# Performance work log

Hardware: AMD Instinct MI355X
Metric: run time of the kernel (lower is better)

## Reference

```python
import jax, jax.numpy as jnp
import numpy as np

D_I = 1024
D_O = 1024
B = 4
S = 4096

def setup_inputs() -> dict:
    key = jax.random.key(0)
    kx, kq, kk, kv = jax.random.split(key, 4)
    x = jax.random.normal(kx, (B, S, D_I), dtype=jnp.float32)
    # torch Linear(d_i, d_o) weight is [d_o, d_i]; we store transposed [d_i, d_o]
    sc = 1.0 / np.sqrt(D_I)
    Wq = jax.random.uniform(kq, (D_I, D_O), jnp.float32, -sc, sc)
    Wk = jax.random.uniform(kk, (D_I, D_O), jnp.float32, -sc, sc)
    Wv = jax.random.uniform(kv, (D_I, D_O), jnp.float32, -sc, sc)
    return {"x": x, "Wq": Wq, "Wk": Wk, "Wv": Wv}

def reference(x, Wq, Wk, Wv):
    # x: [B, S, d_i]
    q = jnp.einsum('bsd,de->bse', x, Wq)  # [B,S,d_o]
    k = jnp.einsum('bsd,de->bse', x, Wk)
    v = jnp.einsum('bsd,de->bse', x, Wv)
    scores = jnp.einsum('bqe,bke->bqk', q, k)  # [B,S,S]
    S_len = x.shape[1]
    causal = jnp.tril(jnp.ones((S_len, S_len), dtype=bool))  # keep lower tri
    scores = jnp.where(causal[None], scores, -jnp.inf)
    attn = jax.nn.softmax(scores / jnp.sqrt(jnp.float32(v.shape[-1])), axis=-1)
    # dropout p=0.0 -> identity
    return jnp.einsum('bqk,bke->bqe', attn, v)  # [B,S,d_o]
```

## Files before the change

### kernel.cpp

```cpp
#include <hip/hip_runtime.h>

typedef __bf16 bf16x8 __attribute__((ext_vector_type(8)));
typedef float f32x4 __attribute__((ext_vector_type(4)));

#define B_SZ 4
#define S_SZ 4096
#define D_SZ 1024
#define ELEMS_MAT ((size_t)B_SZ * S_SZ * D_SZ)

#define OFF_Q  ((size_t)0)
#define OFF_K  (ELEMS_MAT)
#define OFF_VT (2 * ELEMS_MAT)
#define ZONE   (3 * ELEMS_MAT)
#define OFF_XB (ZONE)
#define OFF_V  (ZONE + ELEMS_MAT)
#define OFF_WT (ZONE + 2 * ELEMS_MAT)
#define OFF_S  (ZONE)
#define S_BATCH ((size_t)8912896)

#define MFMA16(a, b, c) __builtin_amdgcn_mfma_f32_16x16x32_bf16((a), (b), (c), 0, 0, 0)

static __device__ __forceinline__ unsigned short f2bf(float f) {
  __bf16 h = (__bf16)f;
  return __builtin_bit_cast(unsigned short, h);
}

static __device__ __forceinline__ void async_lds16(const void* g, void* l) {
  __builtin_amdgcn_global_load_lds((__attribute__((address_space(1))) void*)g,
                                   (__attribute__((address_space(3))) void*)l, 16, 0, 0);
}

__global__ void cast_x_kernel(const float* __restrict__ x, unsigned short* __restrict__ xb) {
  size_t i = ((size_t)blockIdx.x * 256 + threadIdx.x) * 8;
  f32x4 a = *(const f32x4*)(x + i);
  f32x4 b = *(const f32x4*)(x + i + 4);
  bf16x8 o;
  o[0] = (__bf16)a[0]; o[1] = (__bf16)a[1]; o[2] = (__bf16)a[2]; o[3] = (__bf16)a[3];
  o[4] = (__bf16)b[0]; o[5] = (__bf16)b[1]; o[6] = (__bf16)b[2]; o[7] = (__bf16)b[3];
  *(bf16x8*)(xb + i) = o;
}

__global__ void cast_wt_kernel(const float* __restrict__ Wq, const float* __restrict__ Wk,
                               const float* __restrict__ Wv, unsigned short* __restrict__ Wt) {
  __shared__ float tl[64][65];
  const float* W = blockIdx.z == 0 ? Wq : (blockIdx.z == 1 ? Wk : Wv);
  unsigned short* out = Wt + (size_t)blockIdx.z * (size_t)D_SZ * (size_t)D_SZ;
  const int k0 = blockIdx.x * 64, n0 = blockIdx.y * 64;
  const int t = threadIdx.x;
  for (int i = t; i < 4096; i += 256) {
    int r = i >> 6, c = i & 63;
    tl[r][c] = W[(size_t)(k0 + r) * D_SZ + n0 + c];
  }
  __syncthreads();
  for (int i = t; i < 4096; i += 256) {
    int r = i >> 6, c = i & 63;
    out[(size_t)(n0 + r) * D_SZ + k0 + c] = f2bf(tl[c][r]);
  }
}

static __device__ __forceinline__ void stage_tile(const char* Asrc, size_t lda,
                                                  const char* Bsrc, size_t ldb,
                                                  unsigned short* ldsA, unsigned short* ldsB,
                                                  int tid) {
#pragma unroll
  for (int it = 0; it < 4; ++it) {
    int i = it * 512 + tid;
    int row = i >> 3;
    int scol = ((i & 7) ^ (row & 7)) << 4;
    async_lds16(Asrc + (size_t)row * lda + scol, (char*)ldsA + i * 16);
  }
#pragma unroll
  for (int it = 0; it < 4; ++it) {
    int i = it * 512 + tid;
    int row = i >> 3;
    int scol = ((i & 7) ^ (row & 7)) << 4;
    async_lds16(Bsrc + (size_t)row * ldb + scol, (char*)ldsB + i * 16);
  }
}

static __device__ __forceinline__ void compute_tile(const unsigned short* As,
                                                    const unsigned short* Bs,
                                                    int wm, int wn, int lr, int hi,
                                                    f32x4 acc[8][4]) {
  const char* Ab = (const char*)As;
  const char* Bb = (const char*)Bs;
#pragma unroll
  for (int q = 0; q < 4; ++q) {
    const int qm = q >> 1, qn = q & 1;
    bf16x8 af[4][2], bfr[2][2];
#pragma unroll
    for (int f = 0; f < 4; ++f) {
      const int r = wm * 128 + (qm * 4 + f) * 16 + lr;
#pragma unroll
      for (int kk = 0; kk < 2; ++kk)
        af[f][kk] = *(const bf16x8*)(Ab + r * 128 + ((kk * 64 + hi * 16) ^ ((r & 7) << 4)));
    }
#pragma unroll
    for (int f = 0; f < 2; ++f) {
      const int r = wn * 64 + (qn * 2 + f) * 16 + lr;
#pragma unroll
      for (int kk = 0; kk < 2; ++kk)
        bfr[f][kk] = *(const bf16x8*)(Bb + r * 128 + ((kk * 64 + hi * 16) ^ ((r & 7) << 4)));
    }
    __builtin_amdgcn_s_setprio(1);
#pragma unroll
    for (int kk = 0; kk < 2; ++kk)
#pragma unroll
      for (int f = 0; f < 4; ++f)
#pragma unroll
        for (int g = 0; g < 2; ++g)
          acc[qm * 4 + f][qn * 2 + g] = MFMA16(af[f][kk], bfr[g][kk], acc[qm * 4 + f][qn * 2 + g]);
    __builtin_amdgcn_s_setprio(0);
  }
}

static __device__ __forceinline__ void gemm_mainloop(const char* A, size_t lda,
                                                     const char* B, size_t ldb, int NT,
                                                     unsigned short sm[2][2][16384],
                                                     int tid, f32x4 acc[8][4]) {
  const int lane = tid & 63, w = tid >> 6;
  const int wm = w >> 2, wn = w & 3, lr = lane & 15, hi = lane >> 4;
  stage_tile(A, lda, B, ldb, sm[0][0], sm[0][1], tid);
  for (int t = 0; t < NT - 1; ++t) {
    const int cur = t & 1;
    stage_tile(A + (size_t)(t + 1) * 128, lda, B + (size_t)(t + 1) * 128, ldb,
               sm[cur ^ 1][0], sm[cur ^ 1][1], tid);
    asm volatile("s_waitcnt vmcnt(8)" ::: "memory");
    __builtin_amdgcn_s_barrier();
    compute_tile(sm[cur][0], sm[cur][1], wm, wn, lr, hi, acc);
    __builtin_amdgcn_s_barrier();
  }
  asm volatile("s_waitcnt vmcnt(0)" ::: "memory");
  __builtin_amdgcn_s_barrier();
  compute_tile(sm[(NT - 1) & 1][0], sm[(NT - 1) & 1][1], wm, wn, lr, hi, acc);
}

#define GEMM_PRE()                                    \
  __shared__ unsigned short sm[2][2][16384];          \
  const int tid = threadIdx.x;                        \
  f32x4 acc[8][4];                                    \
  {                                                   \
    const f32x4 z4 = {0.f, 0.f, 0.f, 0.f};            \
    _Pragma("unroll") for (int f = 0; f < 8; ++f)     \
      _Pragma("unroll") for (int g = 0; g < 4; ++g)   \
        acc[f][g] = z4;                               \
  }

#define EPI_IDX()                                     \
  const int lane = tid & 63, w = tid >> 6;            \
  const int wm = w >> 2, wn = w & 3;                  \
  const int lr = lane & 15, hi = lane >> 4;

__global__ __launch_bounds__(512, 2) void gemm_qkv256(const unsigned short* __restrict__ xb,
                                                      const unsigned short* __restrict__ Wt,
                                                      unsigned short* __restrict__ Q,
                                                      unsigned short* __restrict__ K,
                                                      unsigned short* __restrict__ V) {
  GEMM_PRE();
  const int bid = blockIdx.x;
  const int sw = (bid & 7) * 96 + (bid >> 3);
  const int mt = sw % 64, nt = sw / 64;
  const char* A = (const char*)xb + (size_t)mt * 256 * 2048;
  const char* Bp = (const char*)Wt + (size_t)nt * 256 * 2048;
  gemm_mainloop(A, 2048, Bp, 2048, 16, sm, tid, acc);
  EPI_IDX();
  unsigned short* Out = (nt >> 2) == 0 ? Q : ((nt >> 2) == 1 ? K : V);
  const int nb = (nt & 3) * 256;
#pragma unroll
  for (int f = 0; f < 8; ++f)
#pragma unroll
    for (int g = 0; g < 4; ++g)
#pragma unroll
      for (int j = 0; j < 4; ++j) {
        const int m = mt * 256 + wm * 128 + f * 16 + hi * 4 + j;
        const int n = nb + wn * 64 + g * 16 + lr;
        Out[(size_t)m * D_SZ + n] = f2bf(acc[f][g][j]);
      }
}

__global__ void transpose_v_kernel(const unsigned short* __restrict__ V,
                                   unsigned short* __restrict__ Vt) {
  __shared__ unsigned short tl[64][65];
  const int s0 = blockIdx.x * 64, d0 = blockIdx.y * 64, b = blockIdx.z;
  const int t = threadIdx.x;
  const unsigned short* Vb = V + (size_t)b * S_SZ * D_SZ;
  unsigned short* Vo = Vt + (size_t)b * D_SZ * S_SZ;
  for (int i = t; i < 4096; i += 256) {
    int r = i >> 6, c = i & 63;
    tl[r][c] = Vb[(size_t)(s0 + r) * D_SZ + d0 + c];
  }
  __syncthreads();
  for (int i = t; i < 4096; i += 256) {
    int r = i >> 6, c = i & 63;
    Vo[(size_t)(d0 + r) * S_SZ + s0 + c] = tl[c][r];
  }
}

__global__ __launch_bounds__(512, 2) void s_gemm256(const unsigned short* __restrict__ Q,
                                                    const unsigned short* __restrict__ K,
                                                    unsigned short* __restrict__ Sp) {
  GEMM_PRE();
  const int bid = blockIdx.x;
  const int sw = (bid & 7) * 68 + (bid >> 3);
  const int b = sw / 136;
  const int tile = sw % 136;
  int I = (int)((sqrtf(8.0f * tile + 1.0f) - 1.0f) * 0.5f);
  while ((I + 1) * (I + 2) / 2 <= tile) ++I;
  while (I * (I + 1) / 2 > tile) --I;
  const int J = tile - I * (I + 1) / 2;
  const char* A = (const char*)Q + ((size_t)b * S_SZ + (size_t)I * 256) * 2048;
  const char* Bp = (const char*)K + ((size_t)b * S_SZ + (size_t)J * 256) * 2048;
  gemm_mainloop(A, 2048, Bp, 2048, 16, sm, tid, acc);
  EPI_IDX();
  const int L = (I + 1) * 256;
  unsigned short* So = Sp + (size_t)b * S_BATCH + (size_t)(I * (I + 1) / 2) * 65536;
#pragma unroll
  for (int f = 0; f < 8; ++f)
#pragma unroll
    for (int g = 0; g < 4; ++g)
#pragma unroll
      for (int j = 0; j < 4; ++j) {
        const int m = wm * 128 + f * 16 + hi * 4 + j;
        const int n = J * 256 + wn * 64 + g * 16 + lr;
        float val = acc[f][g][j] * 0.03125f;
        if (n > I * 256 + m) val = -1e30f;
        So[(size_t)m * L + n] = f2bf(val);
      }
}

__global__ __launch_bounds__(256) void softmax_kernel(unsigned short* __restrict__ Sp) {
  const int w = threadIdx.x >> 6, lane = threadIdx.x & 63;
  const int rowflat = blockIdx.x * 4 + w;
  const int rr = 16383 - rowflat;
  const int b = rr >> 12, q = rr & 4095;
  const int I = q >> 8;
  const int L = (I + 1) << 8;
  unsigned short* base = Sp + (size_t)b * S_BATCH + (size_t)(I * (I + 1) / 2) * 65536 +
                         (size_t)(q & 255) * L;
  const int niter = (L + 511) >> 9;
  const __bf16 NEG = (__bf16)(-1e30f);
  bf16x8 v[8];
#pragma unroll
  for (int jt = 0; jt < 8; ++jt) {
    if (jt < niter) {
      const int off = jt * 512 + lane * 8;
      if (off < L) v[jt] = *(const bf16x8*)(base + off);
      else { bf16x8 fz; fz[0]=NEG;fz[1]=NEG;fz[2]=NEG;fz[3]=NEG;fz[4]=NEG;fz[5]=NEG;fz[6]=NEG;fz[7]=NEG; v[jt] = fz; }
    }
  }
  float m = -1e30f;
#pragma unroll
  for (int jt = 0; jt < 8; ++jt)
    if (jt < niter)
#pragma unroll
      for (int e = 0; e < 8; ++e) m = fmaxf(m, (float)v[jt][e]);
  m = fmaxf(m, __shfl_xor(m, 1));  m = fmaxf(m, __shfl_xor(m, 2));
  m = fmaxf(m, __shfl_xor(m, 4));  m = fmaxf(m, __shfl_xor(m, 8));
  m = fmaxf(m, __shfl_xor(m, 16)); m = fmaxf(m, __shfl_xor(m, 32));
  float l = 0.f;
#pragma unroll
  for (int jt = 0; jt < 8; ++jt)
    if (jt < niter)
#pragma unroll
      for (int e = 0; e < 8; ++e) l += __expf((float)v[jt][e] - m);
  l += __shfl_xor(l, 1);  l += __shfl_xor(l, 2);  l += __shfl_xor(l, 4);
  l += __shfl_xor(l, 8);  l += __shfl_xor(l, 16); l += __shfl_xor(l, 32);
  const float rl = 1.0f / l;
#pragma unroll
  for (int jt = 0; jt < 8; ++jt) {
    if (jt < niter) {
      const int off = jt * 512 + lane * 8;
      if (off < L) {
        bf16x8 p;
#pragma unroll
        for (int e = 0; e < 8; ++e) p[e] = (__bf16)(__expf((float)v[jt][e] - m) * rl);
        *(bf16x8*)(base + off) = p;
      }
    }
  }
}

__global__ __launch_bounds__(512, 2) void pv256(const unsigned short* __restrict__ Sp,
                                                const unsigned short* __restrict__ Vt,
                                                float* __restrict__ out) {
  GEMM_PRE();
  const int bid = blockIdx.x;
  const int sw = (bid & 7) * 32 + (bid >> 3);
  const int I = sw >> 4, b = (sw >> 2) & 3, nt = sw & 3;
  const int L = (I + 1) * 256;
  const char* A = (const char*)(Sp + (size_t)b * S_BATCH + (size_t)(I * (I + 1) / 2) * 65536);
  const char* Bp = (const char*)Vt + ((size_t)b * D_SZ + (size_t)nt * 256) * (S_SZ * 2);
  gemm_mainloop(A, (size_t)L * 2, Bp, S_SZ * 2, (I + 1) * 4, sm, tid, acc);
  EPI_IDX();
#pragma unroll
  for (int f = 0; f < 8; ++f)
#pragma unroll
    for (int g = 0; g < 4; ++g)
#pragma unroll
      for (int j = 0; j < 4; ++j) {
        const int m = wm * 128 + f * 16 + hi * 4 + j;
        const int n = nt * 256 + wn * 64 + g * 16 + lr;
        out[((size_t)b * S_SZ + (size_t)I * 256 + m) * D_SZ + n] = acc[f][g][j];
      }
}

extern "C" void kernel_launch(void* const* d_in, const int* in_sizes, int n_in,
                              void* d_out, int out_size, void* d_ws, size_t ws_size,
                              hipStream_t stream) {
  (void)in_sizes; (void)n_in; (void)out_size; (void)ws_size;
  const float* x  = (const float*)d_in[0];
  const float* Wq = (const float*)d_in[1];
  const float* Wk = (const float*)d_in[2];
  const float* Wv = (const float*)d_in[3];
  float* out = (float*)d_out;
  unsigned short* ws = (unsigned short*)d_ws;

  cast_x_kernel<<<8192, 256, 0, stream>>>(x, ws + OFF_XB);
  cast_wt_kernel<<<dim3(16, 16, 3), 256, 0, stream>>>(Wq, Wk, Wv, ws + OFF_WT);
  gemm_qkv256<<<768, 512, 0, stream>>>(ws + OFF_XB, ws + OFF_WT,
                                       ws + OFF_Q, ws + OFF_K, ws + OFF_V);
  transpose_v_kernel<<<dim3(64, 16, 4), 256, 0, stream>>>(ws + OFF_V, ws + OFF_VT);
  s_gemm256<<<544, 512, 0, stream>>>(ws + OFF_Q, ws + OFF_K, ws + OFF_S);
  softmax_kernel<<<4096, 256, 0, stream>>>(ws + OFF_S);
  pv256<<<256, 512, 0, stream>>>(ws + OFF_S, ws + OFF_VT, out);
}
```

Baseline: 404.0 us.

## Use 256x128 tiles for score GEMM and load-balance causal PV by pairing row blocks

Switches the QK^T score kernel to a new 256x128 tile mainloop, doubling the block count so the causal triangle is covered with finer granularity. The PV kernel now uses 256x128 output tiles and has each block process row block p and then 15-p sequentially, so every block does the same total K-length work instead of a skewed triangular distribution. This aims to remove tail imbalance and improve CU utilisation. In exchange it uses smaller N tiles with less reuse of A, and adds a sequential second pass per block.

New measurement: 406.3 us. Within noise of the previous version (+0.6%).

```diff
diff --git a/kernel.cpp b/kernel.cpp
--- a/kernel.cpp
+++ b/kernel.cpp
@@ -178,6 +178,84 @@
       }
 }
 
+static __device__ __forceinline__ void stage_a256(const char* src, size_t ld, char* lds, int tid) {
+#pragma unroll
+  for (int it = 0; it < 4; ++it) {
+    int i = it * 512 + tid;
+    int row = i >> 3;
+    int scol = ((i & 7) ^ (row & 7)) << 4;
+    async_lds16(src + (size_t)row * ld + scol, lds + i * 16);
+  }
+}
+static __device__ __forceinline__ void stage_b128(const char* src, size_t ld, char* lds, int tid) {
+#pragma unroll
+  for (int it = 0; it < 2; ++it) {
+    int i = it * 512 + tid;
+    int row = i >> 3;
+    int scol = ((i & 7) ^ (row & 7)) << 4;
+    async_lds16(src + (size_t)row * ld + scol, lds + i * 16);
+  }
+}
+
+static __device__ __forceinline__ void compute_tile128(const unsigned short* As,
+                                                       const unsigned short* Bs,
+                                                       int wm, int wn, int lr, int hi,
+                                                       f32x4 acc[8][2]) {
+  const char* Ab = (const char*)As;
+  const char* Bb = (const char*)Bs;
+  bf16x8 bfr[2][2];
+#pragma unroll
+  for (int g = 0; g < 2; ++g) {
+    const int r = wn * 32 + g * 16 + lr;
+#pragma unroll
+    for (int kk = 0; kk < 2; ++kk)
+      bfr[g][kk] = *(const bf16x8*)(Bb + r * 128 + ((kk * 64 + hi * 16) ^ ((r & 7) << 4)));
+  }
+#pragma unroll
+  for (int p = 0; p < 4; ++p) {
+    bf16x8 af[2][2];
+#pragma unroll
+    for (int f = 0; f < 2; ++f) {
+      const int r = wm * 128 + (p * 2 + f) * 16 + lr;
+#pragma unroll
+      for (int kk = 0; kk < 2; ++kk)
+        af[f][kk] = *(const bf16x8*)(Ab + r * 128 + ((kk * 64 + hi * 16) ^ ((r & 7) << 4)));
+    }
+    __builtin_amdgcn_s_setprio(1);
+#pragma unroll
+    for (int kk = 0; kk < 2; ++kk)
+#pragma unroll
+      for (int f = 0; f < 2; ++f)
+#pragma unroll
+        for (int g = 0; g < 2; ++g)
+          acc[p * 2 + f][g] = MFMA16(af[f][kk], bfr[g][kk], acc[p * 2 + f][g]);
+    __builtin_amdgcn_s_setprio(0);
+  }
+}
+
+static __device__ __forceinline__ void mainloop128(const char* A, size_t lda,
+                                                   const char* B, size_t ldb, int NT,
+                                                   unsigned short (*smA)[16384],
+                                                   unsigned short (*smB)[8192],
+                                                   int tid, f32x4 acc[8][2]) {
+  const int lane = tid & 63, w = tid >> 6;
+  const int wm = w >> 2, wn = w & 3, lr = lane & 15, hi = lane >> 4;
+  stage_a256(A, lda, (char*)smA[0], tid);
+  stage_b128(B, ldb, (char*)smB[0], tid);
+  for (int t = 0; t < NT - 1; ++t) {
+    const int cur = t & 1;
+    stage_a256(A + (size_t)(t + 1) * 128, lda, (char*)smA[cur ^ 1], tid);
+    stage_b128(B + (size_t)(t + 1) * 128, ldb, (char*)smB[cur ^ 1], tid);
+    asm volatile("s_waitcnt vmcnt(6)" ::: "memory");
+    __builtin_amdgcn_s_barrier();
+    compute_tile128(smA[cur], smB[cur], wm, wn, lr, hi, acc);
+    __builtin_amdgcn_s_barrier();
+  }
+  asm volatile("s_waitcnt vmcnt(0)" ::: "memory");
+  __builtin_amdgcn_s_barrier();
+  compute_tile128(smA[(NT - 1) & 1], smB[(NT - 1) & 1], wm, wn, lr, hi, acc);
+}
+
 __global__ void transpose_v_kernel(const unsigned short* __restrict__ V,
                                    unsigned short* __restrict__ Vt) {
   __shared__ unsigned short tl[64][65];
@@ -196,32 +274,43 @@
   }
 }
 
-__global__ __launch_bounds__(512, 2) void s_gemm256(const unsigned short* __restrict__ Q,
-                                                    const unsigned short* __restrict__ K,
-                                                    unsigned short* __restrict__ Sp) {
-  GEMM_PRE();
+__global__ __launch_bounds__(512, 2) void s_gemm_bn128(const unsigned short* __restrict__ Q,
+                                                       const unsigned short* __restrict__ K,
+                                                       unsigned short* __restrict__ Sp) {
+  __shared__ unsigned short smA[2][16384];
+  __shared__ unsigned short smB[2][8192];
+  const int tid = threadIdx.x;
+  f32x4 acc[8][2];
+  {
+    const f32x4 z4 = {0.f, 0.f, 0.f, 0.f};
+#pragma unroll
+    for (int f = 0; f < 8; ++f)
+#pragma unroll
+      for (int g = 0; g < 2; ++g) acc[f][g] = z4;
+  }
   const int bid = blockIdx.x;
-  const int sw = (bid & 7) * 68 + (bid >> 3);
-  const int b = sw / 136;
-  const int tile = sw % 136;
-  int I = (int)((sqrtf(8.0f * tile + 1.0f) - 1.0f) * 0.5f);
-  while ((I + 1) * (I + 2) / 2 <= tile) ++I;
-  while (I * (I + 1) / 2 > tile) --I;
-  const int J = tile - I * (I + 1) / 2;
+  const int sw = (bid & 7) * 136 + (bid >> 3);
+  const int b = sw / 272;
+  const int r = sw % 272;
+  int I = (int)((sqrtf(4.0f * r + 1.0f) - 1.0f) * 0.5f);
+  while ((I + 1) * (I + 2) <= r) ++I;
+  while (I * (I + 1) > r) --I;
+  const int Jh = r - I * (I + 1);
+
   const char* A = (const char*)Q + ((size_t)b * S_SZ + (size_t)I * 256) * 2048;
-  const char* Bp = (const char*)K + ((size_t)b * S_SZ + (size_t)J * 256) * 2048;
-  gemm_mainloop(A, 2048, Bp, 2048, 16, sm, tid, acc);
+  const char* Bp = (const char*)K + ((size_t)b * S_SZ + (size_t)Jh * 128) * 2048;
+  mainloop128(A, 2048, Bp, 2048, 16, smA, smB, tid, acc);
   EPI_IDX();
   const int L = (I + 1) * 256;
   unsigned short* So = Sp + (size_t)b * S_BATCH + (size_t)(I * (I + 1) / 2) * 65536;
 #pragma unroll
   for (int f = 0; f < 8; ++f)
 #pragma unroll
-    for (int g = 0; g < 4; ++g)
+    for (int g = 0; g < 2; ++g)
 #pragma unroll
       for (int j = 0; j < 4; ++j) {
         const int m = wm * 128 + f * 16 + hi * 4 + j;
-        const int n = J * 256 + wn * 64 + g * 16 + lr;
+        const int n = Jh * 128 + wn * 32 + g * 16 + lr;
         float val = acc[f][g][j] * 0.03125f;
         if (n > I * 256 + m) val = -1e30f;
         So[(size_t)m * L + n] = f2bf(val);
@@ -280,28 +369,43 @@
   }
 }
 
-__global__ __launch_bounds__(512, 2) void pv256(const unsigned short* __restrict__ Sp,
-                                                const unsigned short* __restrict__ Vt,
-                                                float* __restrict__ out) {
-  GEMM_PRE();
+__global__ __launch_bounds__(512, 2) void pv_bal(const unsigned short* __restrict__ Sp,
+                                                 const unsigned short* __restrict__ Vt,
+                                                 float* __restrict__ out) {
+  __shared__ unsigned short smA[2][16384];
+  __shared__ unsigned short smB[2][8192];
+  const int tid = threadIdx.x;
   const int bid = blockIdx.x;
   const int sw = (bid & 7) * 32 + (bid >> 3);
-  const int I = sw >> 4, b = (sw >> 2) & 3, nt = sw & 3;
-  const int L = (I + 1) * 256;
-  const char* A = (const char*)(Sp + (size_t)b * S_BATCH + (size_t)(I * (I + 1) / 2) * 65536);
-  const char* Bp = (const char*)Vt + ((size_t)b * D_SZ + (size_t)nt * 256) * (S_SZ * 2);
-  gemm_mainloop(A, (size_t)L * 2, Bp, S_SZ * 2, (I + 1) * 4, sm, tid, acc);
+  const int p = sw >> 5, b = (sw >> 3) & 3, nt = sw & 7;
   EPI_IDX();
-#pragma unroll
-  for (int f = 0; f < 8; ++f)
-#pragma unroll
-    for (int g = 0; g < 4; ++g)
-#pragma unroll
-      for (int j = 0; j < 4; ++j) {
-        const int m = wm * 128 + f * 16 + hi * 4 + j;
-        const int n = nt * 256 + wn * 64 + g * 16 + lr;
-        out[((size_t)b * S_SZ + (size_t)I * 256 + m) * D_SZ + n] = acc[f][g][j];
-      }
+  f32x4 acc[8][2];
+#pragma unroll
+  for (int half = 0; half < 2; ++half) {
+    const int I = half ? (15 - p) : p;
+    {
+      const f32x4 z4 = {0.f, 0.f, 0.f, 0.f};
+#pragma unroll
+      for (int f = 0; f < 8; ++f)
+#pragma unroll
+        for (int g = 0; g < 2; ++g) acc[f][g] = z4;
+    }
+    const char* A = (const char*)(Sp + (size_t)b * S_BATCH + (size_t)(I * (I + 1) / 2) * 65536);
+    const size_t lda = (size_t)(I + 1) * 512;
+    const char* Bp = (const char*)Vt + ((size_t)b * D_SZ + (size_t)nt * 128) * (S_SZ * 2);
+    mainloop128(A, lda, Bp, S_SZ * 2, (I + 1) * 4, smA, smB, tid, acc);
+#pragma unroll
+    for (int f = 0; f < 8; ++f)
+#pragma unroll
+      for (int g = 0; g < 2; ++g)
+#pragma unroll
+        for (int j = 0; j < 4; ++j) {
+          const int m = wm * 128 + f * 16 + hi * 4 + j;
+          const int n = nt * 128 + wn * 32 + g * 16 + lr;
+          out[((size_t)b * S_SZ + (size_t)I * 256 + m) * D_SZ + n] = acc[f][g][j];
+        }
+    __syncthreads();
+  }
 }
 
 extern "C" void kernel_launch(void* const* d_in, const int* in_sizes, int n_in,
@@ -320,7 +424,7 @@
   gemm_qkv256<<<768, 512, 0, stream>>>(ws + OFF_XB, ws + OFF_WT,
                                        ws + OFF_Q, ws + OFF_K, ws + OFF_V);
   transpose_v_kernel<<<dim3(64, 16, 4), 256, 0, stream>>>(ws + OFF_V, ws + OFF_VT);
-  s_gemm256<<<544, 512, 0, stream>>>(ws + OFF_Q, ws + OFF_K, ws + OFF_S);
+  s_gemm_bn128<<<1088, 512, 0, stream>>>(ws + OFF_Q, ws + OFF_K, ws + OFF_S);
   softmax_kernel<<<4096, 256, 0, stream>>>(ws + OFF_S);
-  pv256<<<256, 512, 0, stream>>>(ws + OFF_S, ws + OFF_VT, out);
-}
+  pv_bal<<<256, 512, 0, stream>>>(ws + OFF_S, ws + OFF_VT, out);
+}
```

## Pipeline GEMM mainloop in k-halves and load-balance causal PV by pairing row tiles

Applied to the files above, without the earlier changes.

The shared GEMM mainloop now splits each 128-wide k tile into two 64-wide halves staged into separate LDS buffers. Each half is prefetched in phases interleaved with MFMA work, so global-to-LDS copies overlap compute at finer grain. The PV kernel switches to 256x128 output tiles, and each block processes the paired row tiles p and 15-p, equalizing the triangular causal work across blocks. The trade-off is more barriers per k step, a more complex vmcnt accounting that must match issued loads, and smaller per-block tiles in PV.

Measured after the change: 381.9 us. 5.5% less time.

```diff
diff --git a/kernel.cpp b/kernel.cpp
--- a/kernel.cpp
+++ b/kernel.cpp
@@ -58,85 +58,103 @@
   }
 }
 
-static __device__ __forceinline__ void stage_tile(const char* Asrc, size_t lda,
-                                                  const char* Bsrc, size_t ldb,
-                                                  unsigned short* ldsA, unsigned short* ldsB,
-                                                  int tid) {
-#pragma unroll
-  for (int it = 0; it < 4; ++it) {
+static __device__ __forceinline__ bf16x8 lds_frag(const char* half, int r, int hi) {
+  return *(const bf16x8*)(half + r * 64 + ((hi * 16) ^ (((r >> 1) & 3) << 4)));
+}
+
+static __device__ __forceinline__ void stage_half256(const char* src, size_t ld, char* lds, int tid) {
+#pragma unroll
+  for (int it = 0; it < 2; ++it) {
     int i = it * 512 + tid;
-    int row = i >> 3;
-    int scol = ((i & 7) ^ (row & 7)) << 4;
-    async_lds16(Asrc + (size_t)row * lda + scol, (char*)ldsA + i * 16);
-  }
-#pragma unroll
-  for (int it = 0; it < 4; ++it) {
-    int i = it * 512 + tid;
-    int row = i >> 3;
-    int scol = ((i & 7) ^ (row & 7)) << 4;
-    async_lds16(Bsrc + (size_t)row * ldb + scol, (char*)ldsB + i * 16);
-  }
-}
-
-static __device__ __forceinline__ void compute_tile(const unsigned short* As,
-                                                    const unsigned short* Bs,
-                                                    int wm, int wn, int lr, int hi,
-                                                    f32x4 acc[8][4]) {
-  const char* Ab = (const char*)As;
-  const char* Bb = (const char*)Bs;
-#pragma unroll
-  for (int q = 0; q < 4; ++q) {
-    const int qm = q >> 1, qn = q & 1;
-    bf16x8 af[4][2], bfr[2][2];
-#pragma unroll
-    for (int f = 0; f < 4; ++f) {
-      const int r = wm * 128 + (qm * 4 + f) * 16 + lr;
-#pragma unroll
-      for (int kk = 0; kk < 2; ++kk)
-        af[f][kk] = *(const bf16x8*)(Ab + r * 128 + ((kk * 64 + hi * 16) ^ ((r & 7) << 4)));
-    }
-#pragma unroll
-    for (int f = 0; f < 2; ++f) {
-      const int r = wn * 64 + (qn * 2 + f) * 16 + lr;
-#pragma unroll
-      for (int kk = 0; kk < 2; ++kk)
-        bfr[f][kk] = *(const bf16x8*)(Bb + r * 128 + ((kk * 64 + hi * 16) ^ ((r & 7) << 4)));
-    }
-    __builtin_amdgcn_s_setprio(1);
-#pragma unroll
-    for (int kk = 0; kk < 2; ++kk)
-#pragma unroll
-      for (int f = 0; f < 4; ++f)
-#pragma unroll
-        for (int g = 0; g < 2; ++g)
-          acc[qm * 4 + f][qn * 2 + g] = MFMA16(af[f][kk], bfr[g][kk], acc[qm * 4 + f][qn * 2 + g]);
-    __builtin_amdgcn_s_setprio(0);
-  }
-}
-
-static __device__ __forceinline__ void gemm_mainloop(const char* A, size_t lda,
-                                                     const char* B, size_t ldb, int NT,
-                                                     unsigned short sm[2][2][16384],
-                                                     int tid, f32x4 acc[8][4]) {
+    int row = i >> 2;
+    int s = (i & 3) ^ ((row >> 1) & 3);
+    async_lds16(src + (size_t)row * ld + s * 16, lds + i * 16);
+  }
+}
+static __device__ __forceinline__ void stage_half128(const char* src, size_t ld, char* lds, int tid) {
+  int row = tid >> 2;
+  int s = (tid & 3) ^ ((row >> 1) & 3);
+  async_lds16(src + (size_t)row * ld + s * 16, lds + tid * 16);
+}
+
+static __device__ __forceinline__ void mainloop8p(const char* A, size_t lda,
+                                                  const char* B, size_t ldb, int NT,
+                                                  char sm[2][2][2][16384],
+                                                  int tid, f32x4 acc[8][4]) {
   const int lane = tid & 63, w = tid >> 6;
   const int wm = w >> 2, wn = w & 3, lr = lane & 15, hi = lane >> 4;
-  stage_tile(A, lda, B, ldb, sm[0][0], sm[0][1], tid);
-  for (int t = 0; t < NT - 1; ++t) {
-    const int cur = t & 1;
-    stage_tile(A + (size_t)(t + 1) * 128, lda, B + (size_t)(t + 1) * 128, ldb,
-               sm[cur ^ 1][0], sm[cur ^ 1][1], tid);
-    asm volatile("s_waitcnt vmcnt(8)" ::: "memory");
-    __builtin_amdgcn_s_barrier();
-    compute_tile(sm[cur][0], sm[cur][1], wm, wn, lr, hi, acc);
-    __builtin_amdgcn_s_barrier();
-  }
-  asm volatile("s_waitcnt vmcnt(0)" ::: "memory");
+  stage_half256(A,      lda, sm[0][0][0], tid);
+  stage_half256(B,      ldb, sm[0][1][0], tid);
+  stage_half256(A + 64, lda, sm[0][0][1], tid);
+  stage_half256(B + 64, ldb, sm[0][1][1], tid);
+  asm volatile("s_waitcnt vmcnt(4)" ::: "memory");
   __builtin_amdgcn_s_barrier();
-  compute_tile(sm[(NT - 1) & 1][0], sm[(NT - 1) & 1][1], wm, wn, lr, hi, acc);
+  for (int t = 0; t < NT; ++t) {
+    const int d = t & 1;
+    const char* At1 = A + (size_t)(t + 1) * 128;
+    const char* Bt1 = B + (size_t)(t + 1) * 128;
+    const bool pre = (t + 1 < NT);
+    bf16x8 af[4], bfr[4];
+#pragma unroll
+    for (int g = 0; g < 4; ++g) bfr[g] = lds_frag(sm[d][1][0], wn * 64 + g * 16 + lr, hi);
+#pragma unroll
+    for (int f = 0; f < 4; ++f) af[f] = lds_frag(sm[d][0][0], wm * 128 + f * 16 + lr, hi);
+    if (pre) stage_half256(At1, lda, sm[d ^ 1][0][0], tid);
+    __builtin_amdgcn_s_barrier();
+    asm volatile("s_waitcnt lgkmcnt(0)" ::: "memory");
+    __builtin_amdgcn_s_setprio(1);
+#pragma unroll
+    for (int f = 0; f < 4; ++f)
+#pragma unroll
+      for (int g = 0; g < 4; ++g) acc[f][g] = MFMA16(af[f], bfr[g], acc[f][g]);
+    __builtin_amdgcn_s_setprio(0);
+    __builtin_amdgcn_s_barrier();
+#pragma unroll
+    for (int f = 0; f < 4; ++f) af[f] = lds_frag(sm[d][0][0], wm * 128 + 64 + f * 16 + lr, hi);
+    if (pre) stage_half256(Bt1, ldb, sm[d ^ 1][1][0], tid);
+    __builtin_amdgcn_s_barrier();
+    asm volatile("s_waitcnt lgkmcnt(0)" ::: "memory");
+    __builtin_amdgcn_s_setprio(1);
+#pragma unroll
+    for (int f = 0; f < 4; ++f)
+#pragma unroll
+      for (int g = 0; g < 4; ++g) acc[4 + f][g] = MFMA16(af[f], bfr[g], acc[4 + f][g]);
+    __builtin_amdgcn_s_setprio(0);
+    if (pre) asm volatile("s_waitcnt vmcnt(4)" ::: "memory");
+    else     asm volatile("s_waitcnt vmcnt(0)" ::: "memory");
+    __builtin_amdgcn_s_barrier();
+#pragma unroll
+    for (int g = 0; g < 4; ++g) bfr[g] = lds_frag(sm[d][1][1], wn * 64 + g * 16 + lr, hi);
+#pragma unroll
+    for (int f = 0; f < 4; ++f) af[f] = lds_frag(sm[d][0][1], wm * 128 + f * 16 + lr, hi);
+    if (pre) stage_half256(At1 + 64, lda, sm[d ^ 1][0][1], tid);
+    __builtin_amdgcn_s_barrier();
+    asm volatile("s_waitcnt lgkmcnt(0)" ::: "memory");
+    __builtin_amdgcn_s_setprio(1);
+#pragma unroll
+    for (int f = 0; f < 4; ++f)
+#pragma unroll
+      for (int g = 0; g < 4; ++g) acc[f][g] = MFMA16(af[f], bfr[g], acc[f][g]);
+    __builtin_amdgcn_s_setprio(0);
+    __builtin_amdgcn_s_barrier();
+#pragma unroll
+    for (int f = 0; f < 4; ++f) af[f] = lds_frag(sm[d][0][1], wm * 128 + 64 + f * 16 + lr, hi);
+    if (pre) stage_half256(Bt1 + 64, ldb, sm[d ^ 1][1][1], tid);
+    __builtin_amdgcn_s_barrier();
+    asm volatile("s_waitcnt lgkmcnt(0)" ::: "memory");
+    __builtin_amdgcn_s_setprio(1);
+#pragma unroll
+    for (int f = 0; f < 4; ++f)
+#pragma unroll
+      for (int g = 0; g < 4; ++g) acc[4 + f][g] = MFMA16(af[f], bfr[g], acc[4 + f][g]);
+    __builtin_amdgcn_s_setprio(0);
+    if (pre) asm volatile("s_waitcnt vmcnt(4)" ::: "memory");
+    __builtin_amdgcn_s_barrier();
+  }
 }
 
 #define GEMM_PRE()                                    \
-  __shared__ unsigned short sm[2][2][16384];          \
+  __shared__ char sm[2][2][2][16384];                 \
   const int tid = threadIdx.x;                        \
   f32x4 acc[8][4];                                    \
   {                                                   \
@@ -162,7 +180,7 @@
   const int mt = sw % 64, nt = sw / 64;
   const char* A = (const char*)xb + (size_t)mt * 256 * 2048;
   const char* Bp = (const char*)Wt + (size_t)nt * 256 * 2048;
-  gemm_mainloop(A, 2048, Bp, 2048, 16, sm, tid, acc);
+  mainloop8p(A, 2048, Bp, 2048, 16, sm, tid, acc);
   EPI_IDX();
   unsigned short* Out = (nt >> 2) == 0 ? Q : ((nt >> 2) == 1 ? K : V);
   const int nb = (nt & 3) * 256;
@@ -210,7 +228,7 @@
   const int J = tile - I * (I + 1) / 2;
   const char* A = (const char*)Q + ((size_t)b * S_SZ + (size_t)I * 256) * 2048;
   const char* Bp = (const char*)K + ((size_t)b * S_SZ + (size_t)J * 256) * 2048;
-  gemm_mainloop(A, 2048, Bp, 2048, 16, sm, tid, acc);
+  mainloop8p(A, 2048, Bp, 2048, 16, sm, tid, acc);
   EPI_IDX();
   const int L = (I + 1) * 256;
   unsigned short* So = Sp + (size_t)b * S_BATCH + (size_t)(I * (I + 1) / 2) * 65536;
@@ -280,28 +298,98 @@
   }
 }
 
-__global__ __launch_bounds__(512, 2) void pv256(const unsigned short* __restrict__ Sp,
-                                                const unsigned short* __restrict__ Vt,
-                                                float* __restrict__ out) {
-  GEMM_PRE();
+static __device__ __forceinline__ void mainloop2p128(const char* A, size_t lda,
+                                                     const char* B, size_t ldb, int NT,
+                                                     char smA[2][2][16384],
+                                                     char smB[2][2][8192],
+                                                     int tid, f32x4 acc[4][4]) {
+  const int lane = tid & 63, w = tid >> 6;
+  const int wm = w >> 1, wn = w & 1, lr = lane & 15, hi = lane >> 4;
+  stage_half256(A,      lda, smA[0][0], tid);
+  stage_half128(B,      ldb, smB[0][0], tid);
+  stage_half256(A + 64, lda, smA[0][1], tid);
+  stage_half128(B + 64, ldb, smB[0][1], tid);
+  asm volatile("s_waitcnt vmcnt(3)" ::: "memory");
+  __builtin_amdgcn_s_barrier();
+  for (int t = 0; t < NT; ++t) {
+    const int d = t & 1;
+    const char* At1 = A + (size_t)(t + 1) * 128;
+    const char* Bt1 = B + (size_t)(t + 1) * 128;
+    const bool pre = (t + 1 < NT);
+    bf16x8 af[4], bfr[4];
+#pragma unroll
+    for (int g = 0; g < 4; ++g) bfr[g] = lds_frag(smB[d][0], wn * 64 + g * 16 + lr, hi);
+#pragma unroll
+    for (int f = 0; f < 4; ++f) af[f] = lds_frag(smA[d][0], wm * 64 + f * 16 + lr, hi);
+    if (pre) { stage_half256(At1, lda, smA[d ^ 1][0], tid); stage_half128(Bt1, ldb, smB[d ^ 1][0], tid); }
+    __builtin_amdgcn_s_barrier();
+    asm volatile("s_waitcnt lgkmcnt(0)" ::: "memory");
+    __builtin_amdgcn_s_setprio(1);
+#pragma unroll
+    for (int f = 0; f < 4; ++f)
+#pragma unroll
+      for (int g = 0; g < 4; ++g) acc[f][g] = MFMA16(af[f], bfr[g], acc[f][g]);
+    __builtin_amdgcn_s_setprio(0);
+    if (pre) asm volatile("s_waitcnt vmcnt(3)" ::: "memory");
+    else     asm volatile("s_waitcnt vmcnt(0)" ::: "memory");
+    __builtin_amdgcn_s_barrier();
+#pragma unroll
+    for (int g = 0; g < 4; ++g) bfr[g] = lds_frag(smB[d][1], wn * 64 + g * 16 + lr, hi);
+#pragma unroll
+    for (int f = 0; f < 4; ++f) af[f] = lds_frag(smA[d][1], wm * 64 + f * 16 + lr, hi);
+    if (pre) { stage_half256(At1 + 64, lda, smA[d ^ 1][1], tid); stage_half128(Bt1 + 64, ldb, smB[d ^ 1][1], tid); }
+    __builtin_amdgcn_s_barrier();
+    asm volatile("s_waitcnt lgkmcnt(0)" ::: "memory");
+    __builtin_amdgcn_s_setprio(1);
+#pragma unroll
+    for (int f = 0; f < 4; ++f)
+#pragma unroll
+      for (int g = 0; g < 4; ++g) acc[f][g] = MFMA16(af[f], bfr[g], acc[f][g]);
+    __builtin_amdgcn_s_setprio(0);
+    if (pre) asm volatile("s_waitcnt vmcnt(3)" ::: "memory");
+    __builtin_amdgcn_s_barrier();
+  }
+}
+
+__global__ __launch_bounds__(512, 2) void pv_bal(const unsigned short* __restrict__ Sp,
+                                                 const unsigned short* __restrict__ Vt,
+                                                 float* __restrict__ out) {
+  __shared__ char smA[2][2][16384];
+  __shared__ char smB[2][2][8192];
+  const int tid = threadIdx.x;
   const int bid = blockIdx.x;
   const int sw = (bid & 7) * 32 + (bid >> 3);
-  const int I = sw >> 4, b = (sw >> 2) & 3, nt = sw & 3;
-  const int L = (I + 1) * 256;
-  const char* A = (const char*)(Sp + (size_t)b * S_BATCH + (size_t)(I * (I + 1) / 2) * 65536);
-  const char* Bp = (const char*)Vt + ((size_t)b * D_SZ + (size_t)nt * 256) * (S_SZ * 2);
-  gemm_mainloop(A, (size_t)L * 2, Bp, S_SZ * 2, (I + 1) * 4, sm, tid, acc);
-  EPI_IDX();
-#pragma unroll
-  for (int f = 0; f < 8; ++f)
-#pragma unroll
-    for (int g = 0; g < 4; ++g)
-#pragma unroll
-      for (int j = 0; j < 4; ++j) {
-        const int m = wm * 128 + f * 16 + hi * 4 + j;
-        const int n = nt * 256 + wn * 64 + g * 16 + lr;
-        out[((size_t)b * S_SZ + (size_t)I * 256 + m) * D_SZ + n] = acc[f][g][j];
-      }
+  const int p = sw >> 5, b = (sw >> 3) & 3, nt = sw & 7;
+  const int lane = tid & 63, w = tid >> 6;
+  const int wm = w >> 1, wn = w & 1;
+  const int lr = lane & 15, hi = lane >> 4;
+  f32x4 acc[4][4];
+#pragma unroll
+  for (int half = 0; half < 2; ++half) {
+    const int I = half ? (15 - p) : p;
+    {
+      const f32x4 z4 = {0.f, 0.f, 0.f, 0.f};
+#pragma unroll
+      for (int f = 0; f < 4; ++f)
+#pragma unroll
+        for (int g = 0; g < 4; ++g) acc[f][g] = z4;
+    }
+    const char* A = (const char*)(Sp + (size_t)b * S_BATCH + (size_t)(I * (I + 1) / 2) * 65536);
+    const size_t lda = (size_t)(I + 1) * 512;
+    const char* Bp = (const char*)Vt + ((size_t)b * D_SZ + (size_t)nt * 128) * (S_SZ * 2);
+    mainloop2p128(A, lda, Bp, S_SZ * 2, (I + 1) * 4, smA, smB, tid, acc);
+#pragma unroll
+    for (int f = 0; f < 4; ++f)
+#pragma unroll
+      for (int g = 0; g < 4; ++g)
+#pragma unroll
+        for (int j = 0; j < 4; ++j) {
+          const int m = wm * 64 + f * 16 + hi * 4 + j;
+          const int n = nt * 128 + wn * 64 + g * 16 + lr;
+          out[((size_t)b * S_SZ + (size_t)I * 256 + m) * D_SZ + n] = acc[f][g][j];
+        }
+    __syncthreads();
+  }
 }
 
 extern "C" void kernel_launch(void* const* d_in, const int* in_sizes, int n_in,
@@ -322,5 +410,5 @@
   transpose_v_kernel<<<dim3(64, 16, 4), 256, 0, stream>>>(ws + OFF_V, ws + OFF_VT);
   s_gemm256<<<544, 512, 0, stream>>>(ws + OFF_Q, ws + OFF_K, ws + OFF_S);
   softmax_kernel<<<4096, 256, 0, stream>>>(ws + OFF_S);
-  pv256<<<256, 512, 0, stream>>>(ws + OFF_S, ws + OFF_VT, out);
-}
+  pv_bal<<<256, 512, 0, stream>>>(ws + OFF_S, ws + OFF_VT, out);
+}
```
